# Kernel optimization log

Measured on AMD Instinct MI355X. Metric: run time of the kernel, lower is better.

Reference implementation:

```python
import jax, jax.numpy as jnp
import numpy as np
import math

B, T, C = 4, 2048, 2048
N_HEAD = 16
HEAD_DIM = C // N_HEAD

def setup_inputs() -> dict:
    key = jax.random.key(0)
    ks = jax.random.split(key, 11)
    s = 1.0 / math.sqrt(C)
    return {
        "x": jax.random.normal(ks[0], (B, T, C), dtype=jnp.float32),
        "attn_mask": jax.random.normal(ks[1], (B, 1, 1, T), dtype=jnp.float32),
        "Wq": jax.random.normal(ks[2], (C, C), dtype=jnp.float32) * s,
        "bq": jax.random.normal(ks[3], (C,), dtype=jnp.float32) * 0.02,
        "Wk": jax.random.normal(ks[4], (C, C), dtype=jnp.float32) * s,
        "bk": jax.random.normal(ks[5], (C,), dtype=jnp.float32) * 0.02,
        "Wv": jax.random.normal(ks[6], (C, C), dtype=jnp.float32) * s,
        "bv": jax.random.normal(ks[7], (C,), dtype=jnp.float32) * 0.02,
        "Wp": jax.random.normal(ks[8], (C, C), dtype=jnp.float32) * s,
        "bp": jax.random.normal(ks[9], (C,), dtype=jnp.float32) * 0.02,
    }

def reference(x, attn_mask, Wq, bq, Wk, bk, Wv, bv, Wp, bp):
    Bx, Tx, Cx = x.shape
    # QKV projections -> (B, H, T, d)
    q = (x @ Wq.T + bq).reshape(Bx, Tx, N_HEAD, HEAD_DIM).transpose(0, 2, 1, 3)
    k = (x @ Wk.T + bk).reshape(Bx, Tx, N_HEAD, HEAD_DIM).transpose(0, 2, 1, 3)
    v = (x @ Wv.T + bv).reshape(Bx, Tx, N_HEAD, HEAD_DIM).transpose(0, 2, 1, 3)
    scale = 1.0 / math.sqrt(HEAD_DIM)
    att = jnp.einsum('bhqd,bhkd->bhqk', q, k) * scale  # (B,H,T,T)
    causal = jnp.tril(jnp.ones((Tx, Tx), dtype=bool))
    att = jnp.where(causal[None, None], att, -jnp.inf)
    att = att + attn_mask  # additive broadcast mask
    att = jax.nn.softmax(att, axis=-1)
    y = jnp.einsum('bhqk,bhkd->bhqd', att, v)
    y = y.transpose(0, 2, 1, 3).reshape(Bx, Tx, Cx)
    return y @ Wp.T + bp
```

## Files before the change

kernel.cpp:

```cpp
#include <hip/hip_runtime.h>
#include <hip/hip_bf16.h>

#define G1 __attribute__((address_space(1)))
#define L3 __attribute__((address_space(3)))

typedef __bf16 bf16x8 __attribute__((ext_vector_type(8)));
typedef _Float16 half4 __attribute__((ext_vector_type(4)));
typedef float f32x4 __attribute__((ext_vector_type(4)));

#if __has_builtin(__builtin_amdgcn_exp2f)
#define EXP2F(x) __builtin_amdgcn_exp2f(x)
#else
#define EXP2F(x) __expf((x) * 0.69314718056f)
#endif

__device__ __forceinline__ ushort f2bf(float f) {
  union { float f; uint u; } v; v.f = f;
  uint u = v.u;
  u += 0x7fffu + ((u >> 16) & 1u);
  return (ushort)(u >> 16);
}
__device__ __forceinline__ ushort f2h(float f) {
  _Float16 h = (_Float16)f;
  union { _Float16 h; ushort u; } v; v.h = h;
  return v.u;
}

__global__ void cast_bf16_kernel(const float* __restrict__ in, ushort* __restrict__ out, int n4) {
  int i = blockIdx.x * 256 + threadIdx.x;
  if (i >= n4) return;
  float4 v = ((const float4*)in)[i];
  ushort4 o;
  o.x = f2bf(v.x); o.y = f2bf(v.y); o.z = f2bf(v.z); o.w = f2bf(v.w);
  ((ushort4*)out)[i] = o;
}

__global__ void scale_mask_kernel(const float* __restrict__ in, float* __restrict__ out, int n) {
  int i = blockIdx.x * 256 + threadIdx.x;
  if (i < n) out[i] = in[i] * 1.44269504088896f;
}

#define STAGE_A(bf, kt) {                                                       \
    __builtin_amdgcn_global_load_lds((G1 uint*)(Ag0 + (kt) * 32),               \
        (L3 uint*)&As[bf][tid * 8], 16, 0, 0);                                  \
    __builtin_amdgcn_global_load_lds((G1 uint*)(Ag1 + (kt) * 32),               \
        (L3 uint*)&As[bf][4096 + tid * 8], 16, 0, 0);                           \
  }
#define STAGE_B(bf, kt) {                                                       \
    __builtin_amdgcn_global_load_lds((G1 uint*)(Bg0 + (kt) * 32),               \
        (L3 uint*)&Bs[bf][tid * 8], 16, 0, 0);                                  \
    __builtin_amdgcn_global_load_lds((G1 uint*)(Bg1 + (kt) * 32),               \
        (L3 uint*)&Bs[bf][4096 + tid * 8], 16, 0, 0);                           \
  }

template <int MODE>
__global__ __launch_bounds__(512, 2)
void gemm256(const ushort* __restrict__ A,
             const ushort* __restrict__ B0, const ushort* __restrict__ B1,
             const ushort* __restrict__ B2,
             const float* __restrict__ bias0, const float* __restrict__ bias1,
             const float* __restrict__ bias2,
             void* __restrict__ out0, void* __restrict__ out1, void* __restrict__ out2,
             int nbn, int K) {
  __shared__ ushort As[4][8192];
  __shared__ ushort Bs[4][8192];
  const int tid  = threadIdx.x;
  const int wave = tid >> 6, lane = tid & 63;
  const int l15  = lane & 15, quad = lane >> 4;

  const int nwg = gridDim.x;
  const int cpx = nwg >> 3;
  const int swz = (blockIdx.x & 7) * cpx + (blockIdx.x >> 3);
  const int m0 = (swz / nbn) * 256;
  const int n0g = (swz % nbn) * 256;

  int seg = 0, nn = n0g;
  const ushort* Bmat = B0;
  const float* bias = bias0;
  if (MODE == 3) {
    seg = n0g >> 11;
    nn  = n0g & 2047;
    Bmat = seg == 0 ? B0 : (seg == 1 ? B1 : B2);
    bias = seg == 0 ? bias0 : (seg == 1 ? bias1 : bias2);
  }

  const int wm = (wave >> 2) << 7;
  const int wn = (wave & 3) << 6;

  const int fck = (quad ^ ((l15 >> 1) & 3)) << 3;

  const int srow = tid >> 2;
  const int sck  = ((tid & 3) ^ ((srow >> 1) & 3)) * 8;
  const ushort* Ag0 = A    + (size_t)(m0 + srow) * K + sck;
  const ushort* Ag1 = A    + (size_t)(m0 + 128 + srow) * K + sck;
  const ushort* Bg0 = Bmat + (size_t)(nn + srow) * K + sck;
  const ushort* Bg1 = Bmat + (size_t)(nn + 128 + srow) * K + sck;

  f32x4 acc[8][4] = {};

  STAGE_A(0, 0) STAGE_B(0, 0)
  STAGE_A(1, 1) STAGE_B(1, 1)
  STAGE_A(2, 2) STAGE_B(2, 2)
  asm volatile("s_waitcnt vmcnt(8)" ::: "memory");
  __builtin_amdgcn_s_barrier();

  const int NT = K >> 5;
  for (int j = 0; j < NT; j += 4) {
#pragma unroll
    for (int tt = 0; tt < 4; ++tt) {
      const int t   = j + tt;
      const int kt3 = (t + 3) & (NT - 1);
      const int b3  = (tt + 3) & 3;
      bf16x8 bfr[4], af[8];
#pragma unroll
      for (int ni = 0; ni < 4; ++ni)
        bfr[ni] = *(const bf16x8*)&Bs[tt][(wn + ni * 16 + l15) * 32 + fck];
#pragma unroll
      for (int mi = 0; mi < 8; ++mi)
        af[mi] = *(const bf16x8*)&As[tt][(wm + mi * 16 + l15) * 32 + fck];
      STAGE_A(b3, kt3) STAGE_B(b3, kt3)
      __builtin_amdgcn_s_barrier();
      asm volatile("s_waitcnt lgkmcnt(0)" ::: "memory");
      __builtin_amdgcn_s_setprio(1);
#pragma unroll
      for (int mi = 0; mi < 8; ++mi)
#pragma unroll
        for (int ni = 0; ni < 4; ++ni)
          acc[mi][ni] = __builtin_amdgcn_mfma_f32_16x16x32_bf16(af[mi], bfr[ni], acc[mi][ni], 0, 0, 0);
      __builtin_amdgcn_s_setprio(0);
      asm volatile("s_waitcnt vmcnt(8)" ::: "memory");
      __builtin_amdgcn_s_barrier();
    }
  }
  asm volatile("s_waitcnt vmcnt(0)" ::: "memory");

  if (MODE == 3 && seg == 2) {
#pragma unroll
    for (int mi = 0; mi < 8; ++mi)
#pragma unroll
      for (int ni = 0; ni < 4; ++ni) {
        int n = nn + wn + ni * 16 + l15;
        float bv = bias[n];
        int mbase = m0 + wm + mi * 16 + quad * 4;
        int b = mbase >> 11, tq = mbase & 2047, h = n >> 7, dd = n & 127;
        ushort4 o;
        o.x = f2h(acc[mi][ni][0] + bv);
        o.y = f2h(acc[mi][ni][1] + bv);
        o.z = f2h(acc[mi][ni][2] + bv);
        o.w = f2h(acc[mi][ni][3] + bv);
        *(ushort4*)&((ushort*)out2)[(((size_t)(b * 16 + h) * 128 + dd) << 11) + tq] = o;
      }
  } else if (MODE == 3) {
    ushort* dst = seg == 0 ? (ushort*)out0 : (ushort*)out1;
#pragma unroll
    for (int mi = 0; mi < 8; ++mi)
#pragma unroll
      for (int ni = 0; ni < 4; ++ni) {
        int n = nn + wn + ni * 16 + l15;
        float bv = bias[n];
        int mbase = m0 + wm + mi * 16 + quad * 4;
#pragma unroll
        for (int r = 0; r < 4; ++r) {
          int m = mbase + r;
          int b = m >> 11, tq = m & 2047, h = n >> 7, dd = n & 127;
          dst[(((size_t)(b * 16 + h) * 2048 + tq) << 7) + dd] = f2bf(acc[mi][ni][r] + bv);
        }
      }
  } else {
#pragma unroll
    for (int mi = 0; mi < 8; ++mi)
#pragma unroll
      for (int ni = 0; ni < 4; ++ni) {
        int n = n0g + wn + ni * 16 + l15;
        float bv = bias[n];
        int mbase = m0 + wm + mi * 16 + quad * 4;
#pragma unroll
        for (int r = 0; r < 4; ++r)
          ((float*)out0)[(size_t)(mbase + r) * 2048 + n] = acc[mi][ni][r] + bv;
      }
  }
}

__global__ __launch_bounds__(256, 2)
void attn_kernel(const ushort* __restrict__ Q, const ushort* __restrict__ Kh,
                 const ushort* __restrict__ Vt, const float* __restrict__ mask2,
                 ushort* __restrict__ Y) {
  __shared__ ushort Ks[2][8192];
  __shared__ ushort Vs[2][8192];
  const int tid  = threadIdx.x;
  const int wave = tid >> 6, lane = tid & 63;
  const int l15  = lane & 15, quad = lane >> 4;
  const int bh = blockIdx.x;
  const int qt = 15 - blockIdx.y;
  const int b  = bh >> 4, h = bh & 15;
  const int qw0 = qt * 128 + wave * 32;
  const ushort* Qb = Q  + (size_t)bh * 2048 * 128;
  const ushort* Kb = Kh + (size_t)bh * 2048 * 128;
  const ushort* Vb = Vt + (size_t)bh * 128 * 2048;
  const float*  mrow = mask2 + b * 2048;

  bf16x8 aq[2][4];
#pragma unroll
  for (int q2 = 0; q2 < 2; ++q2)
#pragma unroll
    for (int dk = 0; dk < 4; ++dk)
      aq[q2][dk] = *(const bf16x8*)(Qb + (size_t)(qw0 + q2 * 16 + l15) * 128 + dk * 32 + quad * 8);

  auto stageKV = [&](int itn, int bufb) {
    const int k0s = itn * 64;
#pragma unroll
    for (int i = 0; i < 4; ++i) {
      int c = i * 256 + tid;
      int t = c >> 4, ckG = (c & 15) ^ (t & 15);
      __builtin_amdgcn_global_load_lds((G1 uint*)(Kb + (size_t)(k0s + t) * 128 + ckG * 8),
                                       (L3 uint*)&Ks[bufb][c * 8], 16, 0, 0);
    }
#pragma unroll
    for (int i = 0; i < 4; ++i) {
      int c = i * 256 + tid;
      int d = c >> 3, ckG = (c & 7) ^ (d & 7);
      __builtin_amdgcn_global_load_lds((G1 uint*)(Vb + (size_t)d * 2048 + k0s + ckG * 8),
                                       (L3 uint*)&Vs[bufb][c * 8], 16, 0, 0);
    }
  };

  float mi_[2], li[2];
  f32x4 OT[8][2] = {};
  mi_[0] = mi_[1] = -3.0e38f;
  li[0] = li[1] = 0.f;

  const float scale2 = 0.08838834764831845f * 1.44269504088896f;
  const int nkt = 2 * qt + 2;

  stageKV(0, 0);
  for (int it = 0; it < nkt; ++it) {
    const int k0 = it * 64;
    const int bb = it & 1;
    asm volatile("s_waitcnt vmcnt(0)" ::: "memory");
    __builtin_amdgcn_s_barrier();
    if (it + 1 < nkt) stageKV(it + 1, bb ^ 1);

    if (k0 <= qw0 + 31) {
      f32x4 s[2][4] = {};
#pragma unroll
      for (int ns = 0; ns < 4; ++ns) {
        bf16x8 kb[4];
#pragma unroll
        for (int dk = 0; dk < 4; ++dk) {
          int ck = ((dk * 4 + quad) ^ l15);
          kb[dk] = *(const bf16x8*)&Ks[bb][(ns * 16 + l15) * 128 + ck * 8];
        }
#pragma unroll
        for (int q2 = 0; q2 < 2; ++q2)
#pragma unroll
          for (int dk = 0; dk < 4; ++dk)
            s[q2][ns] = __builtin_amdgcn_mfma_f32_16x16x32_bf16(kb[dk], aq[q2][dk], s[q2][ns], 0, 0, 0);
      }

      float4 mk[4];
#pragma unroll
      for (int ns = 0; ns < 4; ++ns)
        mk[ns] = *(const float4*)&mrow[k0 + ns * 16 + quad * 4];

      const bool dmask = (k0 + 63 > qw0);
      half4 pf[2][4];
#pragma unroll
      for (int q2 = 0; q2 < 2; ++q2) {
        const int qr = qw0 + q2 * 16 + l15;
#pragma unroll
        for (int ns = 0; ns < 4; ++ns)
#pragma unroll
          for (int r = 0; r < 4; ++r)
            s[q2][ns][r] = fmaf(s[q2][ns][r], scale2, mk[ns][r]);
        if (dmask) {
#pragma unroll
          for (int ns = 0; ns < 4; ++ns)
#pragma unroll
            for (int r = 0; r < 4; ++r) {
              int kc = k0 + ns * 16 + quad * 4 + r;
              if (kc > qr) s[q2][ns][r] = -3.0e38f;
            }
        }
        float rm = -3.0e38f;
#pragma unroll
        for (int ns = 0; ns < 4; ++ns)
          rm = fmaxf(rm, fmaxf(fmaxf(s[q2][ns][0], s[q2][ns][1]), fmaxf(s[q2][ns][2], s[q2][ns][3])));
        rm = fmaxf(rm, __shfl_xor(rm, 16));
        rm = fmaxf(rm, __shfl_xor(rm, 32));
        const bool skip = __all(rm <= mi_[q2] + 10.0f);
        float mnew = mi_[q2], al = 1.0f;
        if (!skip) {
          mnew = fmaxf(mi_[q2], rm);
          al = EXP2F(mi_[q2] - mnew);
        }
        float rs = 0.f;
#pragma unroll
        for (int ns = 0; ns < 4; ++ns) {
#pragma unroll
          for (int r = 0; r < 4; ++r) {
            float p = EXP2F(s[q2][ns][r] - mnew);
            s[q2][ns][r] = p;
            rs += p;
          }
#if __has_builtin(__builtin_amdgcn_cvt_pkrtz)
          {
            auto lo = __builtin_amdgcn_cvt_pkrtz(s[q2][ns][0], s[q2][ns][1]);
            auto hi = __builtin_amdgcn_cvt_pkrtz(s[q2][ns][2], s[q2][ns][3]);
            pf[q2][ns] = half4{(_Float16)lo[0], (_Float16)lo[1],
                               (_Float16)hi[0], (_Float16)hi[1]};
          }
#else
          pf[q2][ns] = half4{(_Float16)s[q2][ns][0], (_Float16)s[q2][ns][1],
                             (_Float16)s[q2][ns][2], (_Float16)s[q2][ns][3]};
#endif
        }
        rs += __shfl_xor(rs, 16);
        rs += __shfl_xor(rs, 32);
        if (skip) {
          li[q2] += rs;
        } else {
          li[q2] = li[q2] * al + rs;
          mi_[q2] = mnew;
#pragma unroll
          for (int ddt = 0; ddt < 8; ++ddt) OT[ddt][q2] *= al;
        }
      }

#pragma unroll
      for (int ns = 0; ns < 4; ++ns)
#pragma unroll
        for (int ddt = 0; ddt < 8; ++ddt) {
          int row = ddt * 16 + l15;
          int ck = (2 * ns + (quad >> 1)) ^ (l15 & 7);
          half4 vf = *(const half4*)&Vs[bb][row * 64 + ck * 8 + (quad & 1) * 4];
#pragma unroll
          for (int q2 = 0; q2 < 2; ++q2)
            OT[ddt][q2] = __builtin_amdgcn_mfma_f32_16x16x16f16(vf, pf[q2][ns], OT[ddt][q2], 0, 0, 0);
        }
    }
    __builtin_amdgcn_s_barrier();
  }

#pragma unroll
  for (int q2 = 0; q2 < 2; ++q2) {
    float inv = 1.0f / li[q2];
    int t = qw0 + q2 * 16 + l15;
#pragma unroll
    for (int ddt = 0; ddt < 8; ++ddt) {
      ushort4 o;
      o.x = f2bf(OT[ddt][q2][0] * inv);
      o.y = f2bf(OT[ddt][q2][1] * inv);
      o.z = f2bf(OT[ddt][q2][2] * inv);
      o.w = f2bf(OT[ddt][q2][3] * inv);
      *(ushort4*)&Y[((size_t)(b * 2048 + t)) * 2048 + h * 128 + ddt * 16 + quad * 4] = o;
    }
  }
}

extern "C" void kernel_launch(void* const* d_in, const int* in_sizes, int n_in,
                              void* d_out, int out_size, void* d_ws, size_t ws_size,
                              hipStream_t stream) {
  const float* x     = (const float*)d_in[0];
  const float* amask = (const float*)d_in[1];
  const float* Wq = (const float*)d_in[2];
  const float* bq = (const float*)d_in[3];
  const float* Wk = (const float*)d_in[4];
  const float* bk = (const float*)d_in[5];
  const float* Wv = (const float*)d_in[6];
  const float* bv = (const float*)d_in[7];
  const float* Wp = (const float*)d_in[8];
  const float* bp = (const float*)d_in[9];

  char* ws = (char*)d_ws;
  ushort* xb  = (ushort*)(ws);
  ushort* Wqb = (ushort*)(ws + 33554432);
  ushort* Wkb = (ushort*)(ws + 41943040);
  ushort* Wvb = (ushort*)(ws + 50331648);
  ushort* Wpb = (ushort*)(ws + 58720256);
  ushort* Qb  = (ushort*)(ws + 67108864);
  ushort* Kb  = (ushort*)(ws + 100663296);
  ushort* Vtb = (ushort*)(ws + 134217728);
  ushort* Yb  = (ushort*)(ws + 167772160);
  float* mask2 = (float*)d_out;

  cast_bf16_kernel<<<16384, 256, 0, stream>>>(x,  xb,  4194304);
  cast_bf16_kernel<<<4096,  256, 0, stream>>>(Wq, Wqb, 1048576);
  cast_bf16_kernel<<<4096,  256, 0, stream>>>(Wk, Wkb, 1048576);
  cast_bf16_kernel<<<4096,  256, 0, stream>>>(Wv, Wvb, 1048576);
  cast_bf16_kernel<<<4096,  256, 0, stream>>>(Wp, Wpb, 1048576);
  scale_mask_kernel<<<32, 256, 0, stream>>>(amask, mask2, 8192);

  gemm256<3><<<768, 512, 0, stream>>>(xb, Wqb, Wkb, Wvb, bq, bk, bv,
                                      Qb, Kb, Vtb, 24, 2048);

  attn_kernel<<<dim3(64, 16), 256, 0, stream>>>(Qb, Kb, Vtb, mask2, Yb);

  gemm256<2><<<256, 512, 0, stream>>>(Yb, Wpb, nullptr, nullptr, bp, nullptr, nullptr,
                                      d_out, nullptr, nullptr, 8, 2048);
}
```

Measured before the change: 565.9 us.

## Restructure GEMM mainloop to K=64 double-buffered tiles with split phases

Replaces the 4-stage K=32 LDS ring with two 256x64 buffers per operand and splits each K tile into four phases of two M-rows each. Global-to-LDS loads are spread across the phases so copies overlap the MFMA work, and barriers are issued per phase. The swizzle widens to 8 chunks to match the 64-wide rows, and K is hardcoded to 2048. This cuts register pressure for A fragments and halves outer-loop overhead, at the cost of more barriers and less prefetch depth.

```diff
diff --git a/kernel.cpp b/kernel.cpp
--- a/kernel.cpp
+++ b/kernel.cpp
@@ -40,17 +40,35 @@
   if (i < n) out[i] = in[i] * 1.44269504088896f;
 }
 
-#define STAGE_A(bf, kt) {                                                       \
-    __builtin_amdgcn_global_load_lds((G1 uint*)(Ag0 + (kt) * 32),               \
-        (L3 uint*)&As[bf][tid * 8], 16, 0, 0);                                  \
-    __builtin_amdgcn_global_load_lds((G1 uint*)(Ag1 + (kt) * 32),               \
-        (L3 uint*)&As[bf][4096 + tid * 8], 16, 0, 0);                           \
-  }
-#define STAGE_B(bf, kt) {                                                       \
-    __builtin_amdgcn_global_load_lds((G1 uint*)(Bg0 + (kt) * 32),               \
-        (L3 uint*)&Bs[bf][tid * 8], 16, 0, 0);                                  \
-    __builtin_amdgcn_global_load_lds((G1 uint*)(Bg1 + (kt) * 32),               \
-        (L3 uint*)&Bs[bf][4096 + tid * 8], 16, 0, 0);                           \
+#define STG(arr, bf, base, h, kt) {                                              \
+    __builtin_amdgcn_global_load_lds((G1 uint*)((base) + ((h) * 128) * 2048 + (kt) * 64),      \
+        (L3 uint*)&arr[bf][(h) * 8192 + tid * 8], 16, 0, 0);                     \
+    __builtin_amdgcn_global_load_lds((G1 uint*)((base) + ((h) * 128 + 64) * 2048 + (kt) * 64), \
+        (L3 uint*)&arr[bf][(h) * 8192 + 4096 + tid * 8], 16, 0, 0);              \
+  }
+
+#define PHASE(bf, p, STAGES, ENDW) {                                             \
+    if ((p) == 0) {                                                              \
+      _Pragma("unroll") for (int ni = 0; ni < 4; ++ni)                           \
+        _Pragma("unroll") for (int kk = 0; kk < 2; ++kk)                         \
+          bfr[ni][kk] = *(const bf16x8*)&Bs[bf][(wn + ni * 16 + l15) * 64 + fck[kk]]; \
+    }                                                                            \
+    bf16x8 af[2][2];                                                             \
+    _Pragma("unroll") for (int mi2 = 0; mi2 < 2; ++mi2)                          \
+      _Pragma("unroll") for (int kk = 0; kk < 2; ++kk)                           \
+        af[mi2][kk] = *(const bf16x8*)&As[bf][(wm + (2 * (p) + mi2) * 16 + l15) * 64 + fck[kk]]; \
+    STAGES                                                                       \
+    __builtin_amdgcn_s_barrier();                                                \
+    asm volatile("s_waitcnt lgkmcnt(0)" ::: "memory");                           \
+    __builtin_amdgcn_s_setprio(1);                                               \
+    _Pragma("unroll") for (int mi2 = 0; mi2 < 2; ++mi2)                          \
+      _Pragma("unroll") for (int ni = 0; ni < 4; ++ni)                           \
+        _Pragma("unroll") for (int kk = 0; kk < 2; ++kk)                         \
+          acc[2 * (p) + mi2][ni] = __builtin_amdgcn_mfma_f32_16x16x32_bf16(      \
+              af[mi2][kk], bfr[ni][kk], acc[2 * (p) + mi2][ni], 0, 0, 0);        \
+    __builtin_amdgcn_s_setprio(0);                                               \
+    ENDW                                                                         \
+    __builtin_amdgcn_s_barrier();                                                \
   }
 
 template <int MODE>
@@ -61,9 +79,9 @@
              const float* __restrict__ bias0, const float* __restrict__ bias1,
              const float* __restrict__ bias2,
              void* __restrict__ out0, void* __restrict__ out1, void* __restrict__ out2,
-             int nbn, int K) {
-  __shared__ ushort As[4][8192];
-  __shared__ ushort Bs[4][8192];
+             int nbn) {
+  __shared__ ushort As[2][16384];
+  __shared__ ushort Bs[2][16384];
   const int tid  = threadIdx.x;
   const int wave = tid >> 6, lane = tid & 63;
   const int l15  = lane & 15, quad = lane >> 4;
@@ -87,50 +105,34 @@
   const int wm = (wave >> 2) << 7;
   const int wn = (wave & 3) << 6;
 
-  const int fck = (quad ^ ((l15 >> 1) & 3)) << 3;
-
-  const int srow = tid >> 2;
-  const int sck  = ((tid & 3) ^ ((srow >> 1) & 3)) * 8;
-  const ushort* Ag0 = A    + (size_t)(m0 + srow) * K + sck;
-  const ushort* Ag1 = A    + (size_t)(m0 + 128 + srow) * K + sck;
-  const ushort* Bg0 = Bmat + (size_t)(nn + srow) * K + sck;
-  const ushort* Bg1 = Bmat + (size_t)(nn + 128 + srow) * K + sck;
+  const int fck[2] = { ((quad) ^ (l15 & 7)) << 3, ((4 + quad) ^ (l15 & 7)) << 3 };
+
+  const int srow = tid >> 3;
+  const int sck  = ((tid & 7) ^ (srow & 7)) * 8;
+  const ushort* Ag = A    + (size_t)(m0 + srow) * 2048 + sck;
+  const ushort* Bg = Bmat + (size_t)(nn + srow) * 2048 + sck;
 
   f32x4 acc[8][4] = {};
 
-  STAGE_A(0, 0) STAGE_B(0, 0)
-  STAGE_A(1, 1) STAGE_B(1, 1)
-  STAGE_A(2, 2) STAGE_B(2, 2)
-  asm volatile("s_waitcnt vmcnt(8)" ::: "memory");
+  STG(As, 0, Ag, 0, 0) STG(As, 0, Ag, 1, 0)
+  STG(Bs, 0, Bg, 0, 0) STG(Bs, 0, Bg, 1, 0)
+  STG(Bs, 1, Bg, 0, 1) STG(Bs, 1, Bg, 1, 1)
+  asm volatile("s_waitcnt vmcnt(4)" ::: "memory");
   __builtin_amdgcn_s_barrier();
 
-  const int NT = K >> 5;
-  for (int j = 0; j < NT; j += 4) {
-#pragma unroll
-    for (int tt = 0; tt < 4; ++tt) {
-      const int t   = j + tt;
-      const int kt3 = (t + 3) & (NT - 1);
-      const int b3  = (tt + 3) & 3;
-      bf16x8 bfr[4], af[8];
-#pragma unroll
-      for (int ni = 0; ni < 4; ++ni)
-        bfr[ni] = *(const bf16x8*)&Bs[tt][(wn + ni * 16 + l15) * 32 + fck];
-#pragma unroll
-      for (int mi = 0; mi < 8; ++mi)
-        af[mi] = *(const bf16x8*)&As[tt][(wm + mi * 16 + l15) * 32 + fck];
-      STAGE_A(b3, kt3) STAGE_B(b3, kt3)
-      __builtin_amdgcn_s_barrier();
-      asm volatile("s_waitcnt lgkmcnt(0)" ::: "memory");
-      __builtin_amdgcn_s_setprio(1);
-#pragma unroll
-      for (int mi = 0; mi < 8; ++mi)
-#pragma unroll
-        for (int ni = 0; ni < 4; ++ni)
-          acc[mi][ni] = __builtin_amdgcn_mfma_f32_16x16x32_bf16(af[mi], bfr[ni], acc[mi][ni], 0, 0, 0);
-      __builtin_amdgcn_s_setprio(0);
-      asm volatile("s_waitcnt vmcnt(8)" ::: "memory");
-      __builtin_amdgcn_s_barrier();
-    }
+  for (int j = 0; j < 16; ++j) {
+    const int t1 = 2 * j + 1;
+    const int t2 = (2 * j + 2) & 31;
+    const int t3 = (2 * j + 3) & 31;
+    bf16x8 bfr[4][2];
+    PHASE(0, 0, STG(As, 1, Ag, 0, t1), )
+    PHASE(0, 1, STG(As, 1, Ag, 1, t1) STG(Bs, 0, Bg, 0, t2), )
+    PHASE(0, 2, STG(Bs, 0, Bg, 1, t2), )
+    PHASE(0, 3, , asm volatile("s_waitcnt vmcnt(4)" ::: "memory");)
+    PHASE(1, 0, STG(As, 0, Ag, 0, t2), )
+    PHASE(1, 1, STG(As, 0, Ag, 1, t2), )
+    PHASE(1, 2, STG(Bs, 1, Bg, 0, t3), )
+    PHASE(1, 3, STG(Bs, 1, Bg, 1, t3), asm volatile("s_waitcnt vmcnt(4)" ::: "memory");)
   }
   asm volatile("s_waitcnt vmcnt(0)" ::: "memory");
 
@@ -391,10 +393,10 @@
   scale_mask_kernel<<<32, 256, 0, stream>>>(amask, mask2, 8192);
 
   gemm256<3><<<768, 512, 0, stream>>>(xb, Wqb, Wkb, Wvb, bq, bk, bv,
-                                      Qb, Kb, Vtb, 24, 2048);
+                                      Qb, Kb, Vtb, 24);
 
   attn_kernel<<<dim3(64, 16), 256, 0, stream>>>(Qb, Kb, Vtb, mask2, Yb);
 
   gemm256<2><<<256, 512, 0, stream>>>(Yb, Wpb, nullptr, nullptr, bp, nullptr, nullptr,
-                                      d_out, nullptr, nullptr, 8, 2048);
-}
+                                      d_out, nullptr, nullptr, 8);
+}
```

Result: slower. 579.4 us (+2.4%).
